# Kernel optimization log

Measured on AMD Instinct MI355X. Metric: run time of the kernel, lower is better.

## Reference

```python
import jax, jax.numpy as jnp
import numpy as np

KH, KW = 3, 3
K_TERMS = KH * KW + 1  # ones (linear/bias) + 9 shifted patches
# pair indices (i<=j), same ordering as the original layer
_PAIRS = [(i, j) for i in range(K_TERMS) for j in range(i, K_TERMS)]
II = np.array([p[0] for p in _PAIRS])  # [55]
JJ = np.array([p[1] for p in _PAIRS])  # [55]


def setup_inputs() -> dict:
    key = jax.random.key(0)
    k1, k2 = jax.random.split(key)
    B, H, W, C, O = 8, 56, 56, 64, 128
    inputs = jax.random.normal(k1, (B, H, W, C), dtype=jnp.float32)
    # glorot-ish scale for the [1,1,55,C,O] conv3d kernel (squeezed to [55,C,O])
    fan = 55 * C + O
    kernel = jax.random.normal(k2, (55, C, O), dtype=jnp.float32) * jnp.sqrt(2.0 / fan)
    return {"inputs": inputs, "kernel": kernel}


def reference(inputs, kernel):
    B, H, W, C = inputs.shape
    # 'same' padding for stride 1: pad_total = k - 1, asymmetric split as in TF
    ph, pw = KH - 1, KW - 1
    xp = jnp.pad(inputs, ((0, 0), (ph // 2, ph - ph // 2), (pw // 2, pw - pw // 2), (0, 0)))
    # im2col-style shifted slices, row-major over (r, c) like i//kw, i%kw
    shifts = jnp.stack(
        [xp[:, r:r + H, c:c + W, :] for r in range(KH) for c in range(KW)],
        axis=3,
    )  # [B,H,W,9,C]
    ones = jnp.ones((B, H, W, 1, C), dtype=inputs.dtype)
    S = jnp.concatenate([ones, shifts], axis=3)  # [B,H,W,10,C]
    # pairwise quadratic features (includes bias = ones*ones and linear = ones*shift)
    quad = S[:, :, :, II, :] * S[:, :, :, JJ, :]  # [B,H,W,55,C]
    # 1x1x1 conv3d over depth-55 == contraction over (pair, channel)
    return jnp.einsum('bhwpc,pco->bhwo', quad, kernel)  # [B,H,W,O]
```

## Files before the change

kernel.cpp:

```cpp
#include <hip/hip_runtime.h>


#define CB 8
#define CH 56
#define CW 56
#define CC 64
#define CO 128
#define RS 72

typedef __attribute__((ext_vector_type(8))) _Float16 v8hf;
typedef __attribute__((ext_vector_type(16))) float f16f;
typedef __attribute__((address_space(3))) const _Float16 lds_cf16;

__device__ constexpr int PII[55] = {0,0,0,0,0,0,0,0,0,0, 1,1,1,1,1,1,1,1,1, 2,2,2,2,2,2,2,2,
                                    3,3,3,3,3,3,3, 4,4,4,4,4,4, 5,5,5,5,5, 6,6,6,6, 7,7,7, 8,8, 9};
__device__ constexpr int PJJ[55] = {0,1,2,3,4,5,6,7,8,9, 1,2,3,4,5,6,7,8,9, 2,3,4,5,6,7,8,9,
                                    3,4,5,6,7,8,9, 4,5,6,7,8,9, 5,6,7,8,9, 6,7,8,9, 7,8,9, 8,9, 9};

__global__ __launch_bounds__(256) void prep_kernel(const float* __restrict__ K,
                                                   _Float16* __restrict__ BtF) {
  __shared__ float tile[CC * CO];
  const int p = blockIdx.x;
  const int t = threadIdx.x;
  const float* src = K + (size_t)p * CC * CO;
#pragma unroll
  for (int e = 0; e < 8; ++e) {
    const int idx = t * 4 + e * 1024;
    *(float4*)&tile[idx] = *(const float4*)&src[idx];
  }
  __syncthreads();
#pragma unroll
  for (int e4 = 0; e4 < 4; ++e4) {
    const int idx = e4 * 256 + t;
    const int lane = idx & 63;
    const int nqq = (idx >> 6) & 3;
    const int ksq = idx >> 8;
    const int n = nqq * 32 + (lane & 31);
    const int kb = ksq * 16 + (lane >> 5) * 8;
    _Float16 ov[8];
#pragma unroll
    for (int e = 0; e < 8; ++e)
      ov[e] = (_Float16)tile[(kb + e) * CO + n];
    *(v8hf*)(BtF + ((size_t)p * 1024 + idx) * 8) = *(const v8hf*)ov;
  }
}

__global__ __launch_bounds__(256, 1) void quad_kernel(const float* __restrict__ in,
                                                      const _Float16* __restrict__ BtF,
                                                      float* __restrict__ out) {
  __shared__ _Float16 rowsH[4][64][RS];

  const int t = threadIdx.x;
  const int b = blockIdx.x / (CH / 2);
  const int h0 = (blockIdx.x % (CH / 2)) * 2;

  {
    const int col = t >> 2;
    const int cg = (t & 3) * 16;
    const int w = col - 1;
#pragma unroll
    for (int r = 0; r < 4; ++r) {
      const int hh = h0 + r - 1;
      const bool valid = (hh >= 0) && (hh < CH) && (w >= 0) && (w < CW);
      float4 v0 = make_float4(0.f, 0.f, 0.f, 0.f), v1 = v0, v2 = v0, v3 = v0;
      if (valid) {
        const float* s = in + (((size_t)(b * CH + hh)) * CW + w) * CC + cg;
        v0 = *(const float4*)(s);
        v1 = *(const float4*)(s + 4);
        v2 = *(const float4*)(s + 8);
        v3 = *(const float4*)(s + 12);
      }
      _Float16 pv[16];
      pv[0] = (_Float16)v0.x;  pv[1] = (_Float16)v0.y;  pv[2] = (_Float16)v0.z;  pv[3] = (_Float16)v0.w;
      pv[4] = (_Float16)v1.x;  pv[5] = (_Float16)v1.y;  pv[6] = (_Float16)v1.z;  pv[7] = (_Float16)v1.w;
      pv[8] = (_Float16)v2.x;  pv[9] = (_Float16)v2.y;  pv[10] = (_Float16)v2.z; pv[11] = (_Float16)v2.w;
      pv[12] = (_Float16)v3.x; pv[13] = (_Float16)v3.y; pv[14] = (_Float16)v3.z; pv[15] = (_Float16)v3.w;
      _Float16* d = &rowsH[r][col][cg];
      *(v8hf*)(d) = *(const v8hf*)&pv[0];
      *(v8hf*)(d + 8) = *(const v8hf*)&pv[8];
    }
  }

  const int lane = t & 63;
  const int nq = t >> 6;
  const int ml = lane & 31;
  const int hk = lane >> 5;
  const int h8 = hk * 8;

  f16f acc00, acc01, acc10, acc11;
#pragma unroll
  for (int r = 0; r < 16; ++r) { acc00[r] = 0.f; acc01[r] = 0.f; acc10[r] = 0.f; acc11[r] = 0.f; }

  const _Float16* Bw = BtF + (size_t)(nq * 64 + lane) * 8;
  const v8hf vone = {1, 1, 1, 1, 1, 1, 1, 1};

  lds_cf16* lds3 = (lds_cf16*)&rowsH[0][0][0];

  v8hf ring[11];
#pragma unroll
  for (int p = 0; p < 11; ++p) {
    const _Float16* ba = Bw + (size_t)p * 8192;
    asm volatile("global_load_dwordx4 %0, %1, off" : "=v"(ring[p]) : "v"(ba));
  }

  __syncthreads();

#pragma unroll 1
  for (int ks = 0; ks < 4; ++ks) {
    const int koff = ks * 16 + h8;
    v8hf sv0[12], sv1[12];
#pragma unroll
    for (int rr = 0; rr < 4; ++rr)
#pragma unroll
      for (int dx = 0; dx < 3; ++dx) {
        const int c0 = ml + dx;
        int c1 = 32 + ml + dx; c1 = c1 > 63 ? 63 : c1;
        lds_cf16* p0 = lds3 + (rr * 64 + c0) * RS + koff;
        lds_cf16* p1 = lds3 + (rr * 64 + c1) * RS + koff;
        asm volatile("ds_read_b128 %0, %1" : "=v"(sv0[rr * 3 + dx]) : "v"(p0));
        asm volatile("ds_read_b128 %0, %1" : "=v"(sv1[rr * 3 + dx]) : "v"(p1));
      }
    asm volatile("s_waitcnt lgkmcnt(0)"
                 : "+v"(sv0[0]), "+v"(sv0[1]), "+v"(sv0[2]), "+v"(sv0[3]),
                   "+v"(sv0[4]), "+v"(sv0[5]), "+v"(sv0[6]), "+v"(sv0[7]),
                   "+v"(sv0[8]), "+v"(sv0[9]), "+v"(sv0[10]), "+v"(sv0[11]),
                   "+v"(sv1[0]), "+v"(sv1[1]), "+v"(sv1[2]), "+v"(sv1[3]),
                   "+v"(sv1[4]), "+v"(sv1[5]), "+v"(sv1[6]), "+v"(sv1[7]),
                   "+v"(sv1[8]), "+v"(sv1[9]), "+v"(sv1[10]), "+v"(sv1[11]));

    const int ksn = (ks < 3) ? ks + 1 : 3;
#pragma unroll
    for (int p = 0; p < 55; ++p) {
      asm volatile("s_waitcnt vmcnt(10)" : "+v"(ring[p % 11]));
      const v8hf bb = ring[p % 11];
      {
        const int p2 = (p < 44) ? p + 11 : p - 44;
        const int ks2 = (p < 44) ? ks : ksn;
        const _Float16* ba = Bw + (size_t)p2 * 8192 + ks2 * 2048;
        asm volatile("global_load_dwordx4 %0, %1, off" : "=v"(ring[p % 11]) : "v"(ba));
      }
      const int pi = PII[p], pj = PJJ[p];
      v8hf a00, a01, a10, a11;
      if (pi == 0) {
        if (pj == 0) { a00 = vone; a01 = vone; a10 = vone; a11 = vone; }
        else {
          const int dy = (pj - 1) / 3, dx = (pj - 1) % 3;
          a00 = sv0[dy * 3 + dx];        a01 = sv1[dy * 3 + dx];
          a10 = sv0[(dy + 1) * 3 + dx];  a11 = sv1[(dy + 1) * 3 + dx];
        }
      } else {
        const int dyi = (pi - 1) / 3, dxi = (pi - 1) % 3;
        const int dyj = (pj - 1) / 3, dxj = (pj - 1) % 3;
        a00 = sv0[dyi * 3 + dxi] * sv0[dyj * 3 + dxj];
        a01 = sv1[dyi * 3 + dxi] * sv1[dyj * 3 + dxj];
        a10 = sv0[(dyi + 1) * 3 + dxi] * sv0[(dyj + 1) * 3 + dxj];
        a11 = sv1[(dyi + 1) * 3 + dxi] * sv1[(dyj + 1) * 3 + dxj];
      }
      acc00 = __builtin_amdgcn_mfma_f32_32x32x16_f16(a00, bb, acc00, 0, 0, 0);
      acc01 = __builtin_amdgcn_mfma_f32_32x32x16_f16(a01, bb, acc01, 0, 0, 0);
      acc10 = __builtin_amdgcn_mfma_f32_32x32x16_f16(a10, bb, acc10, 0, 0, 0);
      acc11 = __builtin_amdgcn_mfma_f32_32x32x16_f16(a11, bb, acc11, 0, 0, 0);
    }
  }
  asm volatile("s_waitcnt vmcnt(0)");

#pragma unroll
  for (int rw = 0; rw < 2; ++rw) {
    float* ob = out + ((size_t)(b * CH + h0 + rw) * CW) * CO + nq * 32 + ml;
    const f16f accc0 = rw ? acc10 : acc00;
    const f16f accc1 = rw ? acc11 : acc01;
#pragma unroll
    for (int r = 0; r < 16; ++r) {
      const int wp = (r & 3) + 8 * (r >> 2) + 4 * hk;
      ob[(size_t)wp * CO] = accc0[r];
    }
#pragma unroll
    for (int r = 0; r < 12; ++r) {
      const int wp = 32 + (r & 3) + 8 * (r >> 2) + 4 * hk;
      ob[(size_t)wp * CO] = accc1[r];
    }
  }
}

extern "C" void kernel_launch(void* const* d_in, const int* in_sizes, int n_in,
                              void* d_out, int out_size, void* d_ws, size_t ws_size,
                              hipStream_t stream) {
  const float* in = (const float*)d_in[0];
  const float* K = (const float*)d_in[1];
  float* out = (float*)d_out;
  _Float16* BtF = (_Float16*)d_ws;
  (void)in_sizes; (void)n_in; (void)out_size; (void)ws_size;

  prep_kernel<<<55, 256, 0, stream>>>(K, BtF);
  quad_kernel<<<CB * (CH / 2), 256, 0, stream>>>(in, BtF, out);
}
```

Before: 87.13 us.

## Split channel K-steps across two wave groups with LDS reduction

Doubles the block to 512 threads. Each half of the waves processes half of the channel k-steps, and the partial accumulators are combined through a swizzled LDS buffer before the store. Input staging is redistributed over the larger block. The aim is to double the active waves per CU and shorten the serial MFMA chain per wave. In exchange it adds LDS traffic, a barrier, and register pressure under the tighter launch bounds.

```diff
diff --git a/kernel.cpp b/kernel.cpp
--- a/kernel.cpp
+++ b/kernel.cpp
@@ -45,47 +45,45 @@
   }
 }
 
-__global__ __launch_bounds__(256, 1) void quad_kernel(const float* __restrict__ in,
+__global__ __launch_bounds__(512, 2) void quad_kernel(const float* __restrict__ in,
                                                       const _Float16* __restrict__ BtF,
                                                       float* __restrict__ out) {
   __shared__ _Float16 rowsH[4][64][RS];
+  __shared__ float4 red4[4][64][16];
 
   const int t = threadIdx.x;
   const int b = blockIdx.x / (CH / 2);
   const int h0 = (blockIdx.x % (CH / 2)) * 2;
 
   {
-    const int col = t >> 2;
-    const int cg = (t & 3) * 16;
+    const int col = t >> 3;
+    const int cg = (t & 7) * 8;
     const int w = col - 1;
 #pragma unroll
     for (int r = 0; r < 4; ++r) {
       const int hh = h0 + r - 1;
       const bool valid = (hh >= 0) && (hh < CH) && (w >= 0) && (w < CW);
-      float4 v0 = make_float4(0.f, 0.f, 0.f, 0.f), v1 = v0, v2 = v0, v3 = v0;
+      float4 v0 = make_float4(0.f, 0.f, 0.f, 0.f), v1 = v0;
       if (valid) {
         const float* s = in + (((size_t)(b * CH + hh)) * CW + w) * CC + cg;
         v0 = *(const float4*)(s);
         v1 = *(const float4*)(s + 4);
-        v2 = *(const float4*)(s + 8);
-        v3 = *(const float4*)(s + 12);
-      }
-      _Float16 pv[16];
-      pv[0] = (_Float16)v0.x;  pv[1] = (_Float16)v0.y;  pv[2] = (_Float16)v0.z;  pv[3] = (_Float16)v0.w;
-      pv[4] = (_Float16)v1.x;  pv[5] = (_Float16)v1.y;  pv[6] = (_Float16)v1.z;  pv[7] = (_Float16)v1.w;
-      pv[8] = (_Float16)v2.x;  pv[9] = (_Float16)v2.y;  pv[10] = (_Float16)v2.z; pv[11] = (_Float16)v2.w;
-      pv[12] = (_Float16)v3.x; pv[13] = (_Float16)v3.y; pv[14] = (_Float16)v3.z; pv[15] = (_Float16)v3.w;
-      _Float16* d = &rowsH[r][col][cg];
-      *(v8hf*)(d) = *(const v8hf*)&pv[0];
-      *(v8hf*)(d + 8) = *(const v8hf*)&pv[8];
+      }
+      _Float16 pv[8];
+      pv[0] = (_Float16)v0.x; pv[1] = (_Float16)v0.y; pv[2] = (_Float16)v0.z; pv[3] = (_Float16)v0.w;
+      pv[4] = (_Float16)v1.x; pv[5] = (_Float16)v1.y; pv[6] = (_Float16)v1.z; pv[7] = (_Float16)v1.w;
+      *(v8hf*)&rowsH[r][col][cg] = *(const v8hf*)&pv[0];
     }
   }
 
   const int lane = t & 63;
-  const int nq = t >> 6;
+  const int wv = t >> 6;
+  const int nq = wv & 3;
+  const int kh = wv >> 2;
   const int ml = lane & 31;
   const int hk = lane >> 5;
   const int h8 = hk * 8;
+  const int k0 = kh * 2;
 
   f16f acc00, acc01, acc10, acc11;
 #pragma unroll
@@ -99,14 +97,14 @@
   v8hf ring[11];
 #pragma unroll
   for (int p = 0; p < 11; ++p) {
-    const _Float16* ba = Bw + (size_t)p * 8192;
+    const _Float16* ba = Bw + (size_t)p * 8192 + (size_t)k0 * 2048;
     asm volatile("global_load_dwordx4 %0, %1, off" : "=v"(ring[p]) : "v"(ba));
   }
 
   __syncthreads();
 
 #pragma unroll 1
-  for (int ks = 0; ks < 4; ++ks) {
+  for (int ks = k0; ks < k0 + 2; ++ks) {
     const int koff = ks * 16 + h8;
     v8hf sv0[12], sv1[12];
 #pragma unroll
@@ -128,7 +126,7 @@
                    "+v"(sv1[4]), "+v"(sv1[5]), "+v"(sv1[6]), "+v"(sv1[7]),
                    "+v"(sv1[8]), "+v"(sv1[9]), "+v"(sv1[10]), "+v"(sv1[11]));
 
-    const int ksn = (ks < 3) ? ks + 1 : 3;
+    const int ksn = (ks < k0 + 1) ? ks + 1 : ks;
 #pragma unroll
     for (int p = 0; p < 55; ++p) {
       asm volatile("s_waitcnt vmcnt(10)" : "+v"(ring[p % 11]));
@@ -136,7 +134,7 @@
       {
         const int p2 = (p < 44) ? p + 11 : p - 44;
         const int ks2 = (p < 44) ? ks : ksn;
-        const _Float16* ba = Bw + (size_t)p2 * 8192 + ks2 * 2048;
+        const _Float16* ba = Bw + (size_t)p2 * 8192 + (size_t)ks2 * 2048;
         asm volatile("global_load_dwordx4 %0, %1, off" : "=v"(ring[p % 11]) : "v"(ba));
       }
       const int pi = PII[p], pj = PJJ[p];
@@ -164,6 +162,56 @@
   }
   asm volatile("s_waitcnt vmcnt(0)");
 
+  if (kh == 1) {
+#pragma unroll
+    for (int q = 0; q < 4; ++q) {
+      float4 v;
+      v.x = acc00[q * 4 + 0]; v.y = acc00[q * 4 + 1]; v.z = acc00[q * 4 + 2]; v.w = acc00[q * 4 + 3];
+      red4[nq][lane][(0 + q) ^ (lane & 15)] = v;
+    }
+#pragma unroll
+    for (int q = 0; q < 4; ++q) {
+      float4 v;
+      v.x = acc01[q * 4 + 0]; v.y = acc01[q * 4 + 1]; v.z = acc01[q * 4 + 2]; v.w = acc01[q * 4 + 3];
+      red4[nq][lane][(4 + q) ^ (lane & 15)] = v;
+    }
+#pragma unroll
+    for (int q = 0; q < 4; ++q) {
+      float4 v;
+      v.x = acc10[q * 4 + 0]; v.y = acc10[q * 4 + 1]; v.z = acc10[q * 4 + 2]; v.w = acc10[q * 4 + 3];
+      red4[nq][lane][(8 + q) ^ (lane & 15)] = v;
+    }
+#pragma unroll
+    for (int q = 0; q < 4; ++q) {
+      float4 v;
+      v.x = acc11[q * 4 + 0]; v.y = acc11[q * 4 + 1]; v.z = acc11[q * 4 + 2]; v.w = acc11[q * 4 + 3];
+      red4[nq][lane][(12 + q) ^ (lane & 15)] = v;
+    }
+  }
+  __syncthreads();
+  if (kh == 1) return;
+
+#pragma unroll
+  for (int q = 0; q < 4; ++q) {
+    const float4 v = red4[nq][lane][(0 + q) ^ (lane & 15)];
+    acc00[q * 4 + 0] += v.x; acc00[q * 4 + 1] += v.y; acc00[q * 4 + 2] += v.z; acc00[q * 4 + 3] += v.w;
+  }
+#pragma unroll
+  for (int q = 0; q < 4; ++q) {
+    const float4 v = red4[nq][lane][(4 + q) ^ (lane & 15)];
+    acc01[q * 4 + 0] += v.x; acc01[q * 4 + 1] += v.y; acc01[q * 4 + 2] += v.z; acc01[q * 4 + 3] += v.w;
+  }
+#pragma unroll
+  for (int q = 0; q < 4; ++q) {
+    const float4 v = red4[nq][lane][(8 + q) ^ (lane & 15)];
+    acc10[q * 4 + 0] += v.x; acc10[q * 4 + 1] += v.y; acc10[q * 4 + 2] += v.z; acc10[q * 4 + 3] += v.w;
+  }
+#pragma unroll
+  for (int q = 0; q < 4; ++q) {
+    const float4 v = red4[nq][lane][(12 + q) ^ (lane & 15)];
+    acc11[q * 4 + 0] += v.x; acc11[q * 4 + 1] += v.y; acc11[q * 4 + 2] += v.z; acc11[q * 4 + 3] += v.w;
+  }
+
 #pragma unroll
   for (int rw = 0; rw < 2; ++rw) {
     float* ob = out + ((size_t)(b * CH + h0 + rw) * CW) * CO + nq * 32 + ml;
@@ -192,5 +240,5 @@
   (void)in_sizes; (void)n_in; (void)out_size; (void)ws_size;
 
   prep_kernel<<<55, 256, 0, stream>>>(K, BtF);
-  quad_kernel<<<CB * (CH / 2), 256, 0, stream>>>(in, BtF, out);
+  quad_kernel<<<CB * (CH / 2), 512, 0, stream>>>(in, BtF, out);
 }
```

Result: slower. 137.2 us (+57.5%).

## Split column halves across two wave groups with 512-thread blocks

Applied to the files above, without the earlier changes.

Doubles the block to 512 threads so eight waves share the work: each wave now handles one 32-column half of the output row pair instead of both halves. This halves per-wave accumulators, LDS reads and MFMAs, and raises occupancy and latency hiding per CU. The cost is that each B-weight tile is loaded twice from global/L2, once by each column group, and the block spends more time in barriers.

```diff
diff --git a/kernel.cpp b/kernel.cpp
--- a/kernel.cpp
+++ b/kernel.cpp
@@ -45,7 +45,7 @@
   }
 }
 
-__global__ __launch_bounds__(256, 1) void quad_kernel(const float* __restrict__ in,
+__global__ __launch_bounds__(512, 1) void quad_kernel(const float* __restrict__ in,
                                                       const _Float16* __restrict__ BtF,
                                                       float* __restrict__ out) {
   __shared__ _Float16 rowsH[4][64][RS];
@@ -55,41 +55,38 @@
   const int h0 = (blockIdx.x % (CH / 2)) * 2;
 
   {
-    const int col = t >> 2;
-    const int cg = (t & 3) * 16;
+    const int col = t >> 3;
+    const int cg = (t & 7) * 8;
     const int w = col - 1;
 #pragma unroll
     for (int r = 0; r < 4; ++r) {
       const int hh = h0 + r - 1;
       const bool valid = (hh >= 0) && (hh < CH) && (w >= 0) && (w < CW);
-      float4 v0 = make_float4(0.f, 0.f, 0.f, 0.f), v1 = v0, v2 = v0, v3 = v0;
+      float4 v0 = make_float4(0.f, 0.f, 0.f, 0.f), v1 = v0;
       if (valid) {
         const float* s = in + (((size_t)(b * CH + hh)) * CW + w) * CC + cg;
         v0 = *(const float4*)(s);
         v1 = *(const float4*)(s + 4);
-        v2 = *(const float4*)(s + 8);
-        v3 = *(const float4*)(s + 12);
       }
-      _Float16 pv[16];
-      pv[0] = (_Float16)v0.x;  pv[1] = (_Float16)v0.y;  pv[2] = (_Float16)v0.z;  pv[3] = (_Float16)v0.w;
-      pv[4] = (_Float16)v1.x;  pv[5] = (_Float16)v1.y;  pv[6] = (_Float16)v1.z;  pv[7] = (_Float16)v1.w;
-      pv[8] = (_Float16)v2.x;  pv[9] = (_Float16)v2.y;  pv[10] = (_Float16)v2.z; pv[11] = (_Float16)v2.w;
-      pv[12] = (_Float16)v3.x; pv[13] = (_Float16)v3.y; pv[14] = (_Float16)v3.z; pv[15] = (_Float16)v3.w;
-      _Float16* d = &rowsH[r][col][cg];
-      *(v8hf*)(d) = *(const v8hf*)&pv[0];
-      *(v8hf*)(d + 8) = *(const v8hf*)&pv[8];
+      _Float16 pv[8];
+      pv[0] = (_Float16)v0.x; pv[1] = (_Float16)v0.y; pv[2] = (_Float16)v0.z; pv[3] = (_Float16)v0.w;
+      pv[4] = (_Float16)v1.x; pv[5] = (_Float16)v1.y; pv[6] = (_Float16)v1.z; pv[7] = (_Float16)v1.w;
+      *(v8hf*)&rowsH[r][col][cg] = *(const v8hf*)&pv[0];
     }
   }
 
   const int lane = t & 63;
-  const int nq = t >> 6;
+  const int wv = t >> 6;
+  const int nq = wv & 3;
+  const int ch = wv >> 2;
   const int ml = lane & 31;
   const int hk = lane >> 5;
   const int h8 = hk * 8;
+  const int cb = ch * 32;
 
-  f16f acc00, acc01, acc10, acc11;
+  f16f acc0, acc1;
 #pragma unroll
-  for (int r = 0; r < 16; ++r) { acc00[r] = 0.f; acc01[r] = 0.f; acc10[r] = 0.f; acc11[r] = 0.f; }
+  for (int r = 0; r < 16; ++r) { acc0[r] = 0.f; acc1[r] = 0.f; }
 
   const _Float16* Bw = BtF + (size_t)(nq * 64 + lane) * 8;
   const v8hf vone = {1, 1, 1, 1, 1, 1, 1, 1};
@@ -108,25 +105,20 @@
 #pragma unroll 1
   for (int ks = 0; ks < 4; ++ks) {
     const int koff = ks * 16 + h8;
-    v8hf sv0[12], sv1[12];
+    v8hf sv[12];
 #pragma unroll
     for (int rr = 0; rr < 4; ++rr)
 #pragma unroll
       for (int dx = 0; dx < 3; ++dx) {
-        const int c0 = ml + dx;
-        int c1 = 32 + ml + dx; c1 = c1 > 63 ? 63 : c1;
-        lds_cf16* p0 = lds3 + (rr * 64 + c0) * RS + koff;
-        lds_cf16* p1 = lds3 + (rr * 64 + c1) * RS + koff;
-        asm volatile("ds_read_b128 %0, %1" : "=v"(sv0[rr * 3 + dx]) : "v"(p0));
-        asm volatile("ds_read_b128 %0, %1" : "=v"(sv1[rr * 3 + dx]) : "v"(p1));
+        int c = cb + ml + dx;
+        c = c > 63 ? 63 : c;
+        lds_cf16* p0 = lds3 + (rr * 64 + c) * RS + koff;
+        asm volatile("ds_read_b128 %0, %1" : "=v"(sv[rr * 3 + dx]) : "v"(p0));
       }
     asm volatile("s_waitcnt lgkmcnt(0)"
-                 : "+v"(sv0[0]), "+v"(sv0[1]), "+v"(sv0[2]), "+v"(sv0[3]),
-                   "+v"(sv0[4]), "+v"(sv0[5]), "+v"(sv0[6]), "+v"(sv0[7]),
-                   "+v"(sv0[8]), "+v"(sv0[9]), "+v"(sv0[10]), "+v"(sv0[11]),
-                   "+v"(sv1[0]), "+v"(sv1[1]), "+v"(sv1[2]), "+v"(sv1[3]),
-                   "+v"(sv1[4]), "+v"(sv1[5]), "+v"(sv1[6]), "+v"(sv1[7]),
-                   "+v"(sv1[8]), "+v"(sv1[9]), "+v"(sv1[10]), "+v"(sv1[11]));
+                 : "+v"(sv[0]), "+v"(sv[1]), "+v"(sv[2]), "+v"(sv[3]),
+                   "+v"(sv[4]), "+v"(sv[5]), "+v"(sv[6]), "+v"(sv[7]),
+                   "+v"(sv[8]), "+v"(sv[9]), "+v"(sv[10]), "+v"(sv[11]));
 
     const int ksn = (ks < 3) ? ks + 1 : 3;
 #pragma unroll
@@ -136,48 +128,46 @@
       {
         const int p2 = (p < 44) ? p + 11 : p - 44;
         const int ks2 = (p < 44) ? ks : ksn;
-        const _Float16* ba = Bw + (size_t)p2 * 8192 + ks2 * 2048;
+        const _Float16* ba = Bw + (size_t)p2 * 8192 + (size_t)ks2 * 2048;
         asm volatile("global_load_dwordx4 %0, %1, off" : "=v"(ring[p % 11]) : "v"(ba));
       }
       const int pi = PII[p], pj = PJJ[p];
-      v8hf a00, a01, a10, a11;
+      v8hf a0, a1;
       if (pi == 0) {
-        if (pj == 0) { a00 = vone; a01 = vone; a10 = vone; a11 = vone; }
+        if (pj == 0) { a0 = vone; a1 = vone; }
         else {
           const int dy = (pj - 1) / 3, dx = (pj - 1) % 3;
-          a00 = sv0[dy * 3 + dx];        a01 = sv1[dy * 3 + dx];
-          a10 = sv0[(dy + 1) * 3 + dx];  a11 = sv1[(dy + 1) * 3 + dx];
+          a0 = sv[dy * 3 + dx];
+          a1 = sv[(dy + 1) * 3 + dx];
         }
       } else {
         const int dyi = (pi - 1) / 3, dxi = (pi - 1) % 3;
         const int dyj = (pj - 1) / 3, dxj = (pj - 1) % 3;
-        a00 = sv0[dyi * 3 + dxi] * sv0[dyj * 3 + dxj];
-        a01 = sv1[dyi * 3 + dxi] * sv1[dyj * 3 + dxj];
-        a10 = sv0[(dyi + 1) * 3 + dxi] * sv0[(dyj + 1) * 3 + dxj];
-        a11 = sv1[(dyi + 1) * 3 + dxi] * sv1[(dyj + 1) * 3 + dxj];
+        a0 = sv[dyi * 3 + dxi] * sv[dyj * 3 + dxj];
+        a1 = sv[(dyi + 1) * 3 + dxi] * sv[(dyj + 1) * 3 + dxj];
       }
-      acc00 = __builtin_amdgcn_mfma_f32_32x32x16_f16(a00, bb, acc00, 0, 0, 0);
-      acc01 = __builtin_amdgcn_mfma_f32_32x32x16_f16(a01, bb, acc01, 0, 0, 0);
-      acc10 = __builtin_amdgcn_mfma_f32_32x32x16_f16(a10, bb, acc10, 0, 0, 0);
-      acc11 = __builtin_amdgcn_mfma_f32_32x32x16_f16(a11, bb, acc11, 0, 0, 0);
+      acc0 = __builtin_amdgcn_mfma_f32_32x32x16_f16(a0, bb, acc0, 0, 0, 0);
+      acc1 = __builtin_amdgcn_mfma_f32_32x32x16_f16(a1, bb, acc1, 0, 0, 0);
     }
   }
   asm volatile("s_waitcnt vmcnt(0)");
 
 #pragma unroll
   for (int rw = 0; rw < 2; ++rw) {
-    float* ob = out + ((size_t)(b * CH + h0 + rw) * CW) * CO + nq * 32 + ml;
-    const f16f accc0 = rw ? acc10 : acc00;
-    const f16f accc1 = rw ? acc11 : acc01;
+    float* ob = out + ((size_t)(b * CH + h0 + rw) * CW + cb) * CO + nq * 32 + ml;
+    const f16f accc = rw ? acc1 : acc0;
+    if (ch == 0) {
 #pragma unroll
-    for (int r = 0; r < 16; ++r) {
-      const int wp = (r & 3) + 8 * (r >> 2) + 4 * hk;
-      ob[(size_t)wp * CO] = accc0[r];
-    }
+      for (int r = 0; r < 16; ++r) {
+        const int wp = (r & 3) + 8 * (r >> 2) + 4 * hk;
+        ob[(size_t)wp * CO] = accc[r];
+      }
+    } else {
 #pragma unroll
-    for (int r = 0; r < 12; ++r) {
-      const int wp = 32 + (r & 3) + 8 * (r >> 2) + 4 * hk;
-      ob[(size_t)wp * CO] = accc1[r];
+      for (int r = 0; r < 12; ++r) {
+        const int wp = (r & 3) + 8 * (r >> 2) + 4 * hk;
+        ob[(size_t)wp * CO] = accc[r];
+      }
     }
   }
 }
@@ -192,5 +182,5 @@
   (void)in_sizes; (void)n_in; (void)out_size; (void)ws_size;
 
   prep_kernel<<<55, 256, 0, stream>>>(K, BtF);
-  quad_kernel<<<CB * (CH / 2), 256, 0, stream>>>(in, BtF, out);
+  quad_kernel<<<CB * (CH / 2), 512, 0, stream>>>(in, BtF, out);
 }
```

Result: slower. 103.3 us (+18.6%).

## Stage weight fragments through LDS ring via global_load_lds prefetch

Applied to the files above, without the earlier changes.

Replaces the 11-deep register ring of weight loads with a 26-slot LDS ring filled by direct global-to-LDS loads, each read back into registers one step ahead with ds_read. The deeper prefetch is meant to hide global memory latency of the B operand feeding the MFMAs while freeing VGPRs. It adds LDS traffic and a larger shared footprint, and it depends on hand-written waitcnt ordering across wavefronts without barriers, which risks races or stalls.

```diff
diff --git a/kernel.cpp b/kernel.cpp
--- a/kernel.cpp
+++ b/kernel.cpp
@@ -7,10 +7,14 @@
 #define CC 64
 #define CO 128
 #define RS 72
+#define DSLOT 26
 
 typedef __attribute__((ext_vector_type(8))) _Float16 v8hf;
 typedef __attribute__((ext_vector_type(16))) float f16f;
 typedef __attribute__((address_space(3))) const _Float16 lds_cf16;
+typedef __attribute__((address_space(3))) _Float16 lds_f16;
+typedef const __attribute__((address_space(1))) void* gas_t;
+typedef __attribute__((address_space(3))) void* las_t;
 
 __device__ constexpr int PII[55] = {0,0,0,0,0,0,0,0,0,0, 1,1,1,1,1,1,1,1,1, 2,2,2,2,2,2,2,2,
                                     3,3,3,3,3,3,3, 4,4,4,4,4,4, 5,5,5,5,5, 6,6,6,6, 7,7,7, 8,8, 9};
@@ -49,6 +53,7 @@
                                                       const _Float16* __restrict__ BtF,
                                                       float* __restrict__ out) {
   __shared__ _Float16 rowsH[4][64][RS];
+  __shared__ _Float16 ldsB[DSLOT][4][64][8];
 
   const int t = threadIdx.x;
   const int b = blockIdx.x / (CH / 2);
@@ -95,15 +100,23 @@
   const v8hf vone = {1, 1, 1, 1, 1, 1, 1, 1};
 
   lds_cf16* lds3 = (lds_cf16*)&rowsH[0][0][0];
-
-  v8hf ring[11];
-#pragma unroll
-  for (int p = 0; p < 11; ++p) {
-    const _Float16* ba = Bw + (size_t)p * 8192;
-    asm volatile("global_load_dwordx4 %0, %1, off" : "=v"(ring[p]) : "v"(ba));
+  lds_f16* ldsBw = (lds_f16*)&ldsB[0][nq][0][0];
+  lds_cf16* ldsBrL = (lds_cf16*)&ldsB[0][nq][0][0] + lane * 8;
+
+#pragma unroll
+  for (int s0 = 0; s0 < DSLOT; ++s0) {
+    const _Float16* ga = Bw + (size_t)s0 * 8192;
+    __builtin_amdgcn_global_load_lds((gas_t)ga, (las_t)(ldsBw + s0 * 2048), 16, 0, 0);
   }
 
   __syncthreads();
+
+  v8hf bb_cur, bb_nxt;
+  asm volatile("s_waitcnt vmcnt(25)");
+  asm volatile("ds_read_b128 %0, %1" : "=v"(bb_cur) : "v"(ldsBrL));
+
+  int slR = 1;
+  int slW = 0;
 
 #pragma unroll 1
   for (int ks = 0; ks < 4; ++ks) {
@@ -126,19 +139,24 @@
                    "+v"(sv0[8]), "+v"(sv0[9]), "+v"(sv0[10]), "+v"(sv0[11]),
                    "+v"(sv1[0]), "+v"(sv1[1]), "+v"(sv1[2]), "+v"(sv1[3]),
                    "+v"(sv1[4]), "+v"(sv1[5]), "+v"(sv1[6]), "+v"(sv1[7]),
-                   "+v"(sv1[8]), "+v"(sv1[9]), "+v"(sv1[10]), "+v"(sv1[11]));
-
-    const int ksn = (ks < 3) ? ks + 1 : 3;
+                   "+v"(sv1[8]), "+v"(sv1[9]), "+v"(sv1[10]), "+v"(sv1[11]),
+                   "+v"(bb_cur));
+
 #pragma unroll
     for (int p = 0; p < 55; ++p) {
-      asm volatile("s_waitcnt vmcnt(10)" : "+v"(ring[p % 11]));
-      const v8hf bb = ring[p % 11];
       {
-        const int p2 = (p < 44) ? p + 11 : p - 44;
-        const int ks2 = (p < 44) ? ks : ksn;
-        const _Float16* ba = Bw + (size_t)p2 * 8192 + ks2 * 2048;
-        asm volatile("global_load_dwordx4 %0, %1, off" : "=v"(ring[p % 11]) : "v"(ba));
-      }
+        const int p2 = (p < 29) ? p + 26 : p - 29;
+        const int ks2 = (p < 29) ? ks : ((ks == 3) ? 0 : ks + 1);
+        const _Float16* ga = Bw + (size_t)p2 * 8192 + (size_t)ks2 * 2048;
+        __builtin_amdgcn_global_load_lds((gas_t)ga, (las_t)(ldsBw + slW * 2048), 16, 0, 0);
+      }
+      asm volatile("s_waitcnt vmcnt(25)");
+      {
+        lds_cf16* rp = ldsBrL + slR * 2048;
+        asm volatile("ds_read_b128 %0, %1" : "=v"(bb_nxt) : "v"(rp));
+      }
+      asm volatile("s_waitcnt lgkmcnt(1)" : "+v"(bb_cur));
+
       const int pi = PII[p], pj = PJJ[p];
       v8hf a00, a01, a10, a11;
       if (pi == 0) {
@@ -156,10 +174,14 @@
         a10 = sv0[(dyi + 1) * 3 + dxi] * sv0[(dyj + 1) * 3 + dxj];
         a11 = sv1[(dyi + 1) * 3 + dxi] * sv1[(dyj + 1) * 3 + dxj];
       }
-      acc00 = __builtin_amdgcn_mfma_f32_32x32x16_f16(a00, bb, acc00, 0, 0, 0);
-      acc01 = __builtin_amdgcn_mfma_f32_32x32x16_f16(a01, bb, acc01, 0, 0, 0);
-      acc10 = __builtin_amdgcn_mfma_f32_32x32x16_f16(a10, bb, acc10, 0, 0, 0);
-      acc11 = __builtin_amdgcn_mfma_f32_32x32x16_f16(a11, bb, acc11, 0, 0, 0);
+      acc00 = __builtin_amdgcn_mfma_f32_32x32x16_f16(a00, bb_cur, acc00, 0, 0, 0);
+      acc01 = __builtin_amdgcn_mfma_f32_32x32x16_f16(a01, bb_cur, acc01, 0, 0, 0);
+      acc10 = __builtin_amdgcn_mfma_f32_32x32x16_f16(a10, bb_cur, acc10, 0, 0, 0);
+      acc11 = __builtin_amdgcn_mfma_f32_32x32x16_f16(a11, bb_cur, acc11, 0, 0, 0);
+
+      bb_cur = bb_nxt;
+      slW = slR;
+      slR = (slR == DSLOT - 1) ? 0 : slR + 1;
     }
   }
   asm volatile("s_waitcnt vmcnt(0)");
```

Result: slower. 89.32 us (+2.5%).
